# Performance work log

Measured on AMD Instinct MI355X. Metric: run time of the kernel, lower is better.

Reference implementation:

```python
import jax, jax.numpy as jnp
import numpy as np

# Model constants (match init_kwargs)
H = 256          # hidden_dim
NH = 4           # num_heads
L = 4            # gnn_layers
T = 4            # transformer_layers
KMAX = 10        # k_max for overlap embedding
MAXD = 32        # MAX_DIST
INC = 119        # in_channels (atom vocab)
ED = 5           # edge_dim (bond vocab)
B = 64           # graphs per batch
M_SUB = 32       # subgraphs per graph (m)
KNODE = 32       # nodes per subgraph (k)
S = B * M_SUB    # total subgraphs = 2048
N = S * KNODE    # flattened nodes = 65536
E = 131072       # intra-subgraph directed edges


def _ln(x, g, b):
    mu = x.mean(-1, keepdims=True)
    var = ((x - mu) ** 2).mean(-1, keepdims=True)
    return (x - mu) * jax.lax.rsqrt(var + 1e-5) * g + b


def setup_inputs() -> dict:
    key = jax.random.key(0)
    ks = iter(jax.random.split(key, 24))
    nk = lambda: next(ks)
    rn = lambda k_, shp: 0.02 * jax.random.normal(k_, shp, dtype=jnp.float32)

    x_ids = jax.random.randint(nk(), (N,), 0, INC)
    edge_ids = jax.random.randint(nk(), (E,), 0, ED)
    # intra-subgraph edges: endpoints stay within each block of KNODE nodes
    eps_per = E // S
    base = jnp.repeat(jnp.arange(S) * KNODE, eps_per)
    src = base + jax.random.randint(nk(), (E,), 0, KNODE)
    dst = base + jax.random.randint(nk(), (E,), 0, KNODE)
    ns = jax.random.randint(nk(), (S, KNODE), 0, 500)
    padm = jax.random.uniform(nk(), (S, KNODE)) < 0.1
    nodes_sampled = jnp.where(padm, -1, ns)
    dist = jax.random.randint(nk(), (N,), 0, MAXD + 1)
    lp = -5.0 * jax.random.uniform(nk(), (S,))

    return {
        'x_ids': x_ids, 'edge_ids': edge_ids, 'src': src, 'dst': dst,
        'nodes_sampled': nodes_sampled, 'dist': dist, 'lp': lp,
        'atom_emb': rn(nk(), (INC, H)), 'bond_emb': rn(nk(), (ED, H)),
        'dist_emb': rn(nk(), (MAXD + 1, H)),
        'logp_W': rn(nk(), (H,)), 'logp_b': jnp.zeros((H,)),
        'gnn_eps': jnp.zeros((L,)),
        'gnn_W1': rn(nk(), (L, H, H)), 'gnn_b1': jnp.zeros((L, H)),
        'gnn_W2': rn(nk(), (L, H, H)), 'gnn_b2': jnp.zeros((L, H)),
        'ln1_g': jnp.ones((T, H)), 'ln1_b': jnp.zeros((T, H)),
        'qkv_W': rn(nk(), (T, H, 3 * H)),
        'out_W': rn(nk(), (T, H, H)), 'out_b': jnp.zeros((T, H)),
        'ln2_g': jnp.ones((T, H)), 'ln2_b': jnp.zeros((T, H)),
        'f1_W': rn(nk(), (T, H, 4 * H)), 'f1_b': jnp.zeros((T, 4 * H)),
        'f2_W': rn(nk(), (T, 4 * H, H)), 'f2_b': jnp.zeros((T, H)),
        'lnout_g': jnp.ones((H,)), 'lnout_b': jnp.zeros((H,)),
        'overlap_emb': rn(nk(), (KMAX + 1,)),
        'ht_alpha': jnp.ones(()),
    }


def reference(x_ids, edge_ids, src, dst, nodes_sampled, dist, lp,
              atom_emb, bond_emb, dist_emb, logp_W, logp_b,
              gnn_eps, gnn_W1, gnn_b1, gnn_W2, gnn_b2,
              ln1_g, ln1_b, qkv_W, out_W, out_b, ln2_g, ln2_b,
              f1_W, f1_b, f2_W, f2_b, lnout_g, lnout_b,
              overlap_emb, ht_alpha):
    # ---- flatten / embed node features ----
    valid = (nodes_sampled >= 0).reshape(N)
    valid_f = valid.astype(jnp.float32)[:, None]
    lp = jnp.where(jnp.isfinite(lp), lp, 0.0)
    sub_batch = jnp.arange(N) // KNODE
    dist_c = jnp.clip(dist, 0, MAXD)
    logp_pe = jax.nn.relu(lp[sub_batch][:, None] * logp_W + logp_b)
    h = (atom_emb[x_ids] + dist_emb[dist_c] + logp_pe) * valid_f  # [N,H]
    e = bond_emb[edge_ids]                                        # [E,H]

    # ---- GINE message passing ----
    for l in range(L):
        msg = jax.nn.relu(h[src] + e)                       # [E,H] gather
        agg = jax.ops.segment_sum(msg, dst, num_segments=N) # [N,H] scatter-add
        z = (1.0 + gnn_eps[l]) * h + agg
        z = jax.nn.relu(z @ gnn_W1[l] + gnn_b1[l])
        h = (z @ gnn_W2[l] + gnn_b2[l]) * valid_f

    # ---- pool roots into [B, m, H] tokens ----
    root = jnp.arange(S) * KNODE
    x = h[root].reshape(B, M_SUB, H)
    lp2 = lp.reshape(B, M_SUB)

    # ---- pairwise subgraph overlap bias ----
    nodes = nodes_sampled.reshape(B, M_SUB, KNODE)
    vmask = nodes >= 0
    # eq[b,i,j,ki,kj]: node ki of subgraph i equals node kj of subgraph j
    eq = nodes[:, :, None, :, None] == nodes[:, None, :, None, :]
    overlap = (eq.any(-1) & vmask[:, :, None, :]).sum(-1)  # [B,m,m]
    lp_c = jnp.clip(lp2, -30.0, 0.0)
    bias = overlap_emb[jnp.clip(overlap, 0, KMAX)] - ht_alpha * lp_c[:, None, :]
    bias = bias[:, None]  # [B,1,m,m], broadcast over heads

    # ---- relative-bias transformer ----
    hd = H // NH
    scale = 1.0 / np.sqrt(hd).astype(np.float32)
    for t in range(T):
        r = _ln(x, ln1_g[t], ln1_b[t])
        q, k_, v = jnp.split(r @ qkv_W[t], 3, axis=-1)
        q = q.reshape(B, M_SUB, NH, hd)
        k_ = k_.reshape(B, M_SUB, NH, hd)
        v = v.reshape(B, M_SUB, NH, hd)
        scores = jnp.einsum('bihd,bjhd->bhij', q, k_) * scale + bias
        attn = jax.nn.softmax(scores, axis=-1)
        o = jnp.einsum('bhij,bjhd->bihd', attn, v).reshape(B, M_SUB, H)
        x = x + o @ out_W[t] + out_b[t]
        r2 = _ln(x, ln2_g[t], ln2_b[t])
        x = x + jax.nn.gelu(r2 @ f1_W[t] + f1_b[t], approximate=False) @ f2_W[t] + f2_b[t]

    x = _ln(x, lnout_g, lnout_b)
    # HT-weighted mean over subgraph tokens
    w = jax.nn.softmax(-lp_c, axis=1)
    return (w[:, :, None] * x).sum(1)  # [B,H]
```

## Files before the change

### kernel.cpp

```cpp
#include <hip/hip_runtime.h>
#include <hip/hip_bf16.h>
#include <math.h>

#define HDIM   256
#define NHEAD  4
#define LLAY   4
#define TLAY   4
#define KMAXC  10
#define MAXD   32
#define BATCH  64
#define MSUB   32
#define KNODE  32
#define SSUB   2048
#define NNODE  65536
#define NEDGE  131072
#define EPSPER 64
#define EDN    5
#define BSTR   264

typedef unsigned short u16;
typedef __attribute__((ext_vector_type(8))) short bf16x8;
typedef __attribute__((ext_vector_type(4))) float f32x4;

__device__ __forceinline__ float us2f(u16 u) {
    union { unsigned int i; float f; } x; x.i = ((unsigned int)u) << 16; return x.f;
}
__device__ __forceinline__ u16 f2us(float v) {
    union { float f; unsigned int i; } x; x.f = v;
    unsigned int u = x.i;
    u += 0x7fffu + ((u >> 16) & 1u);
    return (u16)(u >> 16);
}
__device__ __forceinline__ float finite_or_zero(float v) {
    return (v == v && fabsf(v) <= 3.0e38f) ? v : 0.0f;
}
__device__ __forceinline__ void gll16(const u16* g, u16* l) {
    __builtin_amdgcn_global_load_lds(
        (const __attribute__((address_space(1))) unsigned int*)g,
        (__attribute__((address_space(3))) unsigned int*)l, 16, 0, 0);
}

__global__ __launch_bounds__(256) void k_csr(
    const int* __restrict__ src, const int* __restrict__ dst,
    const int* __restrict__ eid, u16* __restrict__ perm, u16* __restrict__ off)
{
    __shared__ int sL[4][64], dL[4][64], eL[4][64];
    int wave = threadIdx.x >> 6, lane = threadIdx.x & 63;
    int sgi = blockIdx.x * 4 + wave;
    sL[wave][lane] = src[sgi * 64 + lane] - sgi * KNODE;
    dL[wave][lane] = dst[sgi * 64 + lane] - sgi * KNODE;
    eL[wave][lane] = eid[sgi * 64 + lane];
    __syncthreads();
    if (lane < 32) {
        int cnt = 0;
        for (int e = 0; e < 64; ++e) cnt += (dL[wave][e] == lane) ? 1 : 0;
        int incl = cnt;
        #pragma unroll
        for (int d = 1; d < 32; d <<= 1) {
            int v = __shfl_up(incl, d, 64);
            if (lane >= d) incl += v;
        }
        int start = incl - cnt;
        off[sgi * 32 + lane] = (u16)start;
        int pos = start;
        for (int e = 0; e < 64; ++e) {
            if (dL[wave][e] == lane) {
                perm[sgi * 64 + pos] = (u16)((sL[wave][e] << 3) | eL[wave][e]);
                ++pos;
            }
        }
    }
}

__global__ __launch_bounds__(256) void k_wtrans(
    const float* __restrict__ W, u16* __restrict__ WT, int K, int N)
{
    __shared__ float til[32][33];
    int k0 = blockIdx.x * 32, n0 = blockIdx.y * 32, s = blockIdx.z;
    const float* Wb = W + (size_t)s * K * N;
    u16* Tb = WT + (size_t)s * N * K;
    int j = threadIdx.x & 31, i0 = threadIdx.x >> 5;
    #pragma unroll
    for (int it = 0; it < 4; ++it) {
        int i = i0 + it * 8;
        til[i][j] = Wb[(size_t)(k0 + i) * N + n0 + j];
    }
    __syncthreads();
    #pragma unroll
    for (int it = 0; it < 4; ++it) {
        int i = i0 + it * 8;
        Tb[(size_t)(n0 + i) * K + k0 + j] = f2us(til[j][i]);
    }
}

__global__ __launch_bounds__(256, 2) void k_gnn4(
    const int* __restrict__ x_ids, const int* __restrict__ dist,
    const int* __restrict__ nodes, const float* __restrict__ lp,
    const float* __restrict__ atom_emb, const float* __restrict__ dist_emb,
    const float* __restrict__ logp_W, const float* __restrict__ logp_b,
    const u16* __restrict__ perm, const u16* __restrict__ off,
    const float* __restrict__ bond_emb, const float* __restrict__ eps_arr,
    const float* __restrict__ b1a, const float* __restrict__ b2a,
    const u16* __restrict__ W1T, const u16* __restrict__ W2T,
    float* __restrict__ x)
{
    __shared__ __align__(16) unsigned char smem[38912];
    u16*   hz    = (u16*)smem;
    float* bondL = (float*)(smem + 32768);
    u16*   permL = (u16*)(smem + 38048);
    u16*   offL  = (u16*)(smem + 38304);
    float* validL= (float*)(smem + 38432);
    float* epsL  = (float*)(smem + 38688);

    int tid = threadIdx.x, lane = tid & 63, wave = tid >> 6;
    int row0 = blockIdx.x * 64;
    int fr = lane & 15, quad = lane >> 4;

    for (int i = tid; i < EDN * BSTR; i += 256) {
        int r = i / BSTR, c = i - r * BSTR;
        bondL[i] = (c < 256) ? bond_emb[r * 256 + c] : 0.f;
    }
    if (tid < 128) permL[tid] = perm[blockIdx.x * 128 + tid];
    if (tid < 64) {
        offL[tid] = off[blockIdx.x * 64 + tid];
        validL[tid] = (nodes[row0 + tid] >= 0) ? 1.0f : 0.0f;
    }
    if (tid < 4) epsL[tid] = eps_arr[tid];

    {
        int m = tid & 63, qd = tid >> 6;
        int rg = row0 + m;
        float valid = (nodes[rg] >= 0) ? 1.0f : 0.0f;
        float lpv = finite_or_zero(lp[rg >> 5]);
        int dc = dist[rg]; dc = dc < 0 ? 0 : (dc > MAXD ? MAXD : dc);
        int xid = x_ids[rg];
        #pragma unroll
        for (int k = 0; k < 8; ++k) {
            int cc = qd * 8 + k, c = cc * 8;
            float4 a0 = *reinterpret_cast<const float4*>(atom_emb + xid * 256 + c);
            float4 a1 = *reinterpret_cast<const float4*>(atom_emb + xid * 256 + c + 4);
            float4 d0 = *reinterpret_cast<const float4*>(dist_emb + dc * 256 + c);
            float4 d1 = *reinterpret_cast<const float4*>(dist_emb + dc * 256 + c + 4);
            float4 w0 = *reinterpret_cast<const float4*>(logp_W + c);
            float4 w1 = *reinterpret_cast<const float4*>(logp_W + c + 4);
            float4 p0 = *reinterpret_cast<const float4*>(logp_b + c);
            float4 p1 = *reinterpret_cast<const float4*>(logp_b + c + 4);
            union { bf16x8 v; ushort4 h[2]; } o;
            o.h[0] = (ushort4){
                f2us((a0.x + d0.x + fmaxf(lpv * w0.x + p0.x, 0.f)) * valid),
                f2us((a0.y + d0.y + fmaxf(lpv * w0.y + p0.y, 0.f)) * valid),
                f2us((a0.z + d0.z + fmaxf(lpv * w0.z + p0.z, 0.f)) * valid),
                f2us((a0.w + d0.w + fmaxf(lpv * w0.w + p0.w, 0.f)) * valid) };
            o.h[1] = (ushort4){
                f2us((a1.x + d1.x + fmaxf(lpv * w1.x + p1.x, 0.f)) * valid),
                f2us((a1.y + d1.y + fmaxf(lpv * w1.y + p1.y, 0.f)) * valid),
                f2us((a1.z + d1.z + fmaxf(lpv * w1.z + p1.z, 0.f)) * valid),
                f2us((a1.w + d1.w + fmaxf(lpv * w1.w + p1.w, 0.f)) * valid) };
            *reinterpret_cast<bf16x8*>(hz + m * 256 + ((cc ^ (m & 7)) * 8)) = o.v;
        }
    }
    __syncthreads();

    int rl = tid >> 3, g8 = tid & 7;
    for (int l = 0; l < LLAY; ++l) {
        float ep1 = 1.0f + epsL[l];
        for (int p = 0; p < 2; ++p) {
            int row = p * 32 + rl;
            int e0 = offL[p * 32 + rl];
            int e1 = (rl < 31) ? offL[p * 32 + rl + 1] : 64;
            float a[32];
            #pragma unroll
            for (int q = 0; q < 32; ++q) a[q] = 0.f;
            for (int j = e0; j < e1; ++j) {
                int ent = permL[p * 64 + j];
                int sl = p * 32 + (ent >> 3);
                int be = ent & 7;
                #pragma unroll
                for (int q = 0; q < 4; ++q) {
                    int cc = q * 8 + g8;
                    union { bf16x8 v; u16 s[8]; } hv;
                    hv.v = *reinterpret_cast<const bf16x8*>(
                        hz + sl * 256 + ((cc ^ (sl & 7)) * 8));
                    const float* bp = bondL + be * BSTR + cc * 8;
                    float4 bo0 = *reinterpret_cast<const float4*>(bp);
                    float4 bo1 = *reinterpret_cast<const float4*>(bp + 4);
                    a[q*8+0] += fmaxf(us2f(hv.s[0]) + bo0.x, 0.f);
                    a[q*8+1] += fmaxf(us2f(hv.s[1]) + bo0.y, 0.f);
                    a[q*8+2] += fmaxf(us2f(hv.s[2]) + bo0.z, 0.f);
                    a[q*8+3] += fmaxf(us2f(hv.s[3]) + bo0.w, 0.f);
                    a[q*8+4] += fmaxf(us2f(hv.s[4]) + bo1.x, 0.f);
                    a[q*8+5] += fmaxf(us2f(hv.s[5]) + bo1.y, 0.f);
                    a[q*8+6] += fmaxf(us2f(hv.s[6]) + bo1.z, 0.f);
                    a[q*8+7] += fmaxf(us2f(hv.s[7]) + bo1.w, 0.f);
                }
            }
            __syncthreads();
            #pragma unroll
            for (int q = 0; q < 4; ++q) {
                int cc = q * 8 + g8;
                u16* ptr = hz + row * 256 + ((cc ^ (row & 7)) * 8);
                union { bf16x8 v; u16 s[8]; } hv, ov;
                hv.v = *reinterpret_cast<const bf16x8*>(ptr);
                #pragma unroll
                for (int k = 0; k < 8; ++k)
                    ov.s[k] = f2us(ep1 * us2f(hv.s[k]) + a[q * 8 + k]);
                *reinterpret_cast<bf16x8*>(ptr) = ov.v;
            }
        }
        __syncthreads();

        const u16* W1 = W1T + l * 65536;
        const float* b1 = b1a + l * 256;
        bf16x8 wf[4][8];
        #pragma unroll
        for (int i = 0; i < 4; ++i)
            #pragma unroll
            for (int kc = 0; kc < 8; ++kc)
                wf[i][kc] = *reinterpret_cast<const bf16x8*>(
                    W1 + (size_t)(wave * 64 + i * 16 + fr) * 256 + kc * 32 + quad * 8);
        f32x4 acc[4][4];
        #pragma unroll
        for (int i = 0; i < 4; ++i)
            #pragma unroll
            for (int j = 0; j < 4; ++j) acc[i][j] = (f32x4){0.f, 0.f, 0.f, 0.f};
        #pragma unroll
        for (int kc = 0; kc < 8; ++kc) {
            bf16x8 bfv[4];
            #pragma unroll
            for (int j = 0; j < 4; ++j) {
                int m = j * 16 + fr;
                bfv[j] = *reinterpret_cast<const bf16x8*>(hz + m * 256 + (((kc * 4 + quad) ^ (m & 7)) * 8));
            }
            #pragma unroll
            for (int i = 0; i < 4; ++i)
                #pragma unroll
                for (int j = 0; j < 4; ++j)
                    acc[i][j] = __builtin_amdgcn_mfma_f32_16x16x32_bf16(wf[i][kc], bfv[j], acc[i][j], 0, 0, 0);
        }
        __syncthreads();
        #pragma unroll
        for (int i = 0; i < 4; ++i) {
            int n1b = wave * 64 + i * 16 + quad * 4;
            float4 bb = *reinterpret_cast<const float4*>(b1 + n1b);
            #pragma unroll
            for (int j = 0; j < 4; ++j) {
                int m = j * 16 + fr;
                ushort4 o = { f2us(fmaxf(acc[i][j][0] + bb.x, 0.f)),
                              f2us(fmaxf(acc[i][j][1] + bb.y, 0.f)),
                              f2us(fmaxf(acc[i][j][2] + bb.z, 0.f)),
                              f2us(fmaxf(acc[i][j][3] + bb.w, 0.f)) };
                *reinterpret_cast<ushort4*>(hz + m * 256 + (((n1b >> 3) ^ (m & 7)) * 8) + (n1b & 7)) = o;
            }
        }
        __syncthreads();

        const u16* W2 = W2T + l * 65536;
        const float* b2 = b2a + l * 256;
        #pragma unroll
        for (int i = 0; i < 4; ++i)
            #pragma unroll
            for (int kc = 0; kc < 8; ++kc)
                wf[i][kc] = *reinterpret_cast<const bf16x8*>(
                    W2 + (size_t)(wave * 64 + i * 16 + fr) * 256 + kc * 32 + quad * 8);
        #pragma unroll
        for (int i = 0; i < 4; ++i)
            #pragma unroll
            for (int j = 0; j < 4; ++j) acc[i][j] = (f32x4){0.f, 0.f, 0.f, 0.f};
        #pragma unroll
        for (int kc = 0; kc < 8; ++kc) {
            bf16x8 bfv[4];
            #pragma unroll
            for (int j = 0; j < 4; ++j) {
                int m = j * 16 + fr;
                bfv[j] = *reinterpret_cast<const bf16x8*>(hz + m * 256 + (((kc * 4 + quad) ^ (m & 7)) * 8));
            }
            #pragma unroll
            for (int i = 0; i < 4; ++i)
                #pragma unroll
                for (int j = 0; j < 4; ++j)
                    acc[i][j] = __builtin_amdgcn_mfma_f32_16x16x32_bf16(wf[i][kc], bfv[j], acc[i][j], 0, 0, 0);
        }
        __syncthreads();

        if (l < LLAY - 1) {
            #pragma unroll
            for (int i = 0; i < 4; ++i) {
                int n2b = wave * 64 + i * 16 + quad * 4;
                float4 bb = *reinterpret_cast<const float4*>(b2 + n2b);
                #pragma unroll
                for (int j = 0; j < 4; ++j) {
                    int m = j * 16 + fr;
                    float vm = validL[m];
                    ushort4 o = { f2us((acc[i][j][0] + bb.x) * vm),
                                  f2us((acc[i][j][1] + bb.y) * vm),
                                  f2us((acc[i][j][2] + bb.z) * vm),
                                  f2us((acc[i][j][3] + bb.w) * vm) };
                    *reinterpret_cast<ushort4*>(hz + m * 256 + (((n2b >> 3) ^ (m & 7)) * 8) + (n2b & 7)) = o;
                }
            }
            __syncthreads();
        } else {
            if (fr == 0) {
                #pragma unroll
                for (int i = 0; i < 4; ++i) {
                    int n2b = wave * 64 + i * 16 + quad * 4;
                    float4 bb = *reinterpret_cast<const float4*>(b2 + n2b);
                    #pragma unroll
                    for (int jj = 0; jj < 2; ++jj) {
                        int j = jj * 2, m = j * 16;
                        float vm = validL[m];
                        float4 o = { (acc[i][j][0] + bb.x) * vm,
                                     (acc[i][j][1] + bb.y) * vm,
                                     (acc[i][j][2] + bb.z) * vm,
                                     (acc[i][j][3] + bb.w) * vm };
                        *reinterpret_cast<float4*>(
                            x + (size_t)(blockIdx.x * 2 + (m >> 5)) * 256 + n2b) = o;
                    }
                }
            }
        }
    }
}

__global__ __launch_bounds__(1024) void k_bias(
    const int* __restrict__ nodes, const float* __restrict__ lp,
    const float* __restrict__ ovl_emb, const float* __restrict__ alpha_p,
    float* __restrict__ bias)
{
    int b = blockIdx.x, tid = threadIdx.x;
    __shared__ int nd[32][32];
    __shared__ unsigned int bmv[32][17];
    __shared__ float lpc[32];
    __shared__ float emb[16];
    nd[tid >> 5][tid & 31] = nodes[b * 1024 + tid];
    if (tid < 512) bmv[tid >> 4][tid & 15] = 0u;
    if (tid < 32) {
        float l = finite_or_zero(lp[b * 32 + tid]);
        l = l < -30.f ? -30.f : (l > 0.f ? 0.f : l);
        lpc[tid] = l;
    }
    if (tid >= 64 && tid < 64 + KMAXC + 1) emb[tid - 64] = ovl_emb[tid - 64];
    __syncthreads();
    int own = nd[tid >> 5][tid & 31];
    if (own >= 0) atomicOr(&bmv[tid >> 5][own >> 5], 1u << (own & 31));
    __syncthreads();
    int i = tid >> 5, j = tid & 31;
    float alpha = alpha_p[0];
    int cnt = 0;
    #pragma unroll
    for (int k = 0; k < 32; ++k) {
        int nk = nd[i][k];
        if (nk >= 0) cnt += (int)((bmv[j][nk >> 5] >> (nk & 31)) & 1u);
    }
    bias[b * 1024 + tid] = emb[cnt > KMAXC ? KMAXC : cnt] - alpha * lpc[j];
}

__global__ __launch_bounds__(256) void k_gemmA_ln(
    const float* __restrict__ X, const u16* __restrict__ BT,
    const float* __restrict__ ln_g, const float* __restrict__ ln_b,
    const float* __restrict__ bias, u16* __restrict__ C,
    int N, int act)
{
    __shared__ __align__(16) u16 As[32 * 256];
    __shared__ __align__(16) u16 Bs[64 * 256];
    int tid = threadIdx.x, lane = tid & 63, wave = tid >> 6;
    int wm = wave >> 1, wn = wave & 1;
    int bm = blockIdx.y * 32, bn = blockIdx.x * 64;
    int fr = lane & 15, quad = lane >> 4;

    #pragma unroll
    for (int t = 0; t < 8; ++t) {
        int v = t * 4 + wave;
        int r = v * 2 + (lane >> 5);
        int p = lane & 31;
        int cc = p ^ (r & 7);
        gll16(BT + (size_t)(bn + r) * 256 + cc * 8, Bs + v * 512);
    }
    #pragma unroll
    for (int rr = 0; rr < 8; ++rr) {
        int r = wave * 8 + rr;
        float4 xv = *reinterpret_cast<const float4*>(X + (size_t)(bm + r) * 256 + lane * 4);
        float s = xv.x + xv.y + xv.z + xv.w;
        #pragma unroll
        for (int o2 = 32; o2 > 0; o2 >>= 1) s += __shfl_xor(s, o2);
        float mu = s * (1.0f / 256.0f);
        float d0 = xv.x - mu, d1 = xv.y - mu, d2 = xv.z - mu, d3 = xv.w - mu;
        float sq = d0 * d0 + d1 * d1 + d2 * d2 + d3 * d3;
        #pragma unroll
        for (int o2 = 32; o2 > 0; o2 >>= 1) sq += __shfl_xor(sq, o2);
        float rs = rsqrtf(sq * (1.0f / 256.0f) + 1e-5f);
        int c = lane * 4;
        float4 gv = *reinterpret_cast<const float4*>(ln_g + c);
        float4 bv = *reinterpret_cast<const float4*>(ln_b + c);
        ushort4 o = { f2us(d0 * rs * gv.x + bv.x), f2us(d1 * rs * gv.y + bv.y),
                      f2us(d2 * rs * gv.z + bv.z), f2us(d3 * rs * gv.w + bv.w) };
        *reinterpret_cast<ushort4*>(As + r * 256 + (((lane >> 1) ^ (r & 7)) * 8) + (lane & 1) * 4) = o;
    }
    __syncthreads();

    f32x4 acc[2];
    acc[0] = (f32x4){0,0,0,0}; acc[1] = (f32x4){0,0,0,0};
    #pragma unroll
    for (int kc = 0; kc < 8; ++kc) {
        int am = wm * 16 + fr;
        bf16x8 af = *reinterpret_cast<const bf16x8*>(
            As + am * 256 + (((kc * 4 + quad) ^ (am & 7)) * 8));
        bf16x8 bfr[2];
        #pragma unroll
        for (int j = 0; j < 2; ++j) {
            int br = wn * 32 + j * 16 + fr;
            bfr[j] = *reinterpret_cast<const bf16x8*>(
                Bs + br * 256 + (((kc * 4 + quad) ^ (br & 7)) * 8));
        }
        acc[0] = __builtin_amdgcn_mfma_f32_16x16x32_bf16(af, bfr[0], acc[0], 0, 0, 0);
        acc[1] = __builtin_amdgcn_mfma_f32_16x16x32_bf16(af, bfr[1], acc[1], 0, 0, 0);
    }
    int crow0 = bm + wm * 16 + quad * 4;
    int ccol0 = bn + wn * 32 + fr;
    #pragma unroll
    for (int r = 0; r < 4; ++r) {
        int m = crow0 + r;
        #pragma unroll
        for (int j = 0; j < 2; ++j) {
            int n = ccol0 + j * 16;
            float v = acc[j][r];
            if (bias) v += bias[n];
            if (act == 2) v = 0.5f * v * (1.0f + erff(v * 0.70710678118654752f));
            C[(size_t)m * N + n] = f2us(v);
        }
    }
}

__global__ __launch_bounds__(256) void k_gemmB(
    const u16* __restrict__ A, const u16* __restrict__ BT,
    const float* __restrict__ bias, float* __restrict__ Cout,
    const float* __restrict__ resid, int M, int K, int N)
{
    __shared__ __align__(16) u16 As[32 * 256];
    __shared__ __align__(16) u16 Bs[64 * 256];
    int tid = threadIdx.x, lane = tid & 63, wave = tid >> 6;
    int wm = wave >> 1, wn = wave & 1;
    int bm = blockIdx.y * 32, bn = blockIdx.x * 64;
    int fr = lane & 15, quad = lane >> 4;
    int npan = K >> 8;

    f32x4 acc[2];
    acc[0] = (f32x4){0,0,0,0}; acc[1] = (f32x4){0,0,0,0};
    for (int pan = 0; pan < npan; ++pan) {
        if (pan) __syncthreads();
        int kbase = pan * 256;
        #pragma unroll
        for (int t = 0; t < 4; ++t) {
            int v = t * 4 + wave;
            int r = v * 2 + (lane >> 5);
            int p = lane & 31;
            int cc = p ^ (r & 7);
            gll16(A + (size_t)(bm + r) * K + kbase + cc * 8, As + v * 512);
        }
        #pragma unroll
        for (int t = 0; t < 8; ++t) {
            int v = t * 4 + wave;
            int r = v * 2 + (lane >> 5);
            int p = lane & 31;
            int cc = p ^ (r & 7);
            gll16(BT + (size_t)(bn + r) * K + kbase + cc * 8, Bs + v * 512);
        }
        __syncthreads();
        #pragma unroll
        for (int kc = 0; kc < 8; ++kc) {
            int am = wm * 16 + fr;
            bf16x8 af = *reinterpret_cast<const bf16x8*>(
                As + am * 256 + (((kc * 4 + quad) ^ (am & 7)) * 8));
            bf16x8 bfr[2];
            #pragma unroll
            for (int j = 0; j < 2; ++j) {
                int br = wn * 32 + j * 16 + fr;
                bfr[j] = *reinterpret_cast<const bf16x8*>(
                    Bs + br * 256 + (((kc * 4 + quad) ^ (br & 7)) * 8));
            }
            acc[0] = __builtin_amdgcn_mfma_f32_16x16x32_bf16(af, bfr[0], acc[0], 0, 0, 0);
            acc[1] = __builtin_amdgcn_mfma_f32_16x16x32_bf16(af, bfr[1], acc[1], 0, 0, 0);
        }
    }
    int crow0 = bm + wm * 16 + quad * 4;
    int ccol0 = bn + wn * 32 + fr;
    #pragma unroll
    for (int r = 0; r < 4; ++r) {
        int m = crow0 + r;
        #pragma unroll
        for (int j = 0; j < 2; ++j) {
            int n = ccol0 + j * 16;
            Cout[(size_t)m * N + n] = acc[j][r] + bias[n] + resid[(size_t)m * N + n];
        }
    }
}

__global__ __launch_bounds__(256) void k_attn(
    const u16* __restrict__ qkv, const float* __restrict__ bias, u16* __restrict__ o)
{
    int b = blockIdx.x >> 2, hh = blockIdx.x & 3;
    __shared__ float qs[32][65], ks[32][65], vs[32][65];
    __shared__ float sc[32][33];
    int tid = threadIdx.x;
    #pragma unroll
    for (int u = 0; u < 8; ++u) {
        int idx = tid + u * 256;
        int i = idx >> 6, d = idx & 63;
        size_t base = (size_t)(b * 32 + i) * 768;
        qs[i][d] = us2f(qkv[base + hh * 64 + d]);
        ks[i][d] = us2f(qkv[base + 256 + hh * 64 + d]);
        vs[i][d] = us2f(qkv[base + 512 + hh * 64 + d]);
    }
    __syncthreads();
    #pragma unroll
    for (int u = 0; u < 4; ++u) {
        int p = tid + u * 256;
        int i = p >> 5, j = p & 31;
        float s = 0.f;
        #pragma unroll
        for (int d = 0; d < 64; ++d) s += qs[i][d] * ks[j][d];
        sc[i][j] = s * 0.125f + bias[b * 1024 + i * 32 + j];
    }
    __syncthreads();
    if (tid < 32) {
        int i = tid;
        float m = -1e30f;
        for (int j = 0; j < 32; ++j) m = fmaxf(m, sc[i][j]);
        float sum = 0.f;
        for (int j = 0; j < 32; ++j) { float e = expf(sc[i][j] - m); sc[i][j] = e; sum += e; }
        float inv = 1.0f / sum;
        for (int j = 0; j < 32; ++j) sc[i][j] *= inv;
    }
    __syncthreads();
    #pragma unroll
    for (int u = 0; u < 8; ++u) {
        int idx = tid + u * 256;
        int i = idx >> 6, d = idx & 63;
        float a = 0.f;
        #pragma unroll
        for (int j = 0; j < 32; ++j) a += sc[i][j] * vs[j][d];
        o[(size_t)(b * 32 + i) * 256 + hh * 64 + d] = f2us(a);
    }
}

__global__ __launch_bounds__(256) void k_fin(
    const float* __restrict__ x, const float* __restrict__ lp,
    const float* __restrict__ lnout_g, const float* __restrict__ lnout_b,
    float* __restrict__ out)
{
    __shared__ __align__(16) float xlnf[32 * 260];
    __shared__ float wfin[32];
    int tid = threadIdx.x, lane = tid & 63, wave = tid >> 6;
    int b = blockIdx.x;
    #pragma unroll
    for (int rr = 0; rr < 8; ++rr) {
        int row = wave * 8 + rr;
        float4 xv = *reinterpret_cast<const float4*>(x + (size_t)(b * 32 + row) * 256 + lane * 4);
        float s = xv.x + xv.y + xv.z + xv.w;
        #pragma unroll
        for (int o2 = 32; o2 > 0; o2 >>= 1) s += __shfl_xor(s, o2);
        float mu = s * (1.0f / 256.0f);
        float d0 = xv.x - mu, d1 = xv.y - mu, d2 = xv.z - mu, d3 = xv.w - mu;
        float sq = d0 * d0 + d1 * d1 + d2 * d2 + d3 * d3;
        #pragma unroll
        for (int o2 = 32; o2 > 0; o2 >>= 1) sq += __shfl_xor(sq, o2);
        float rs = rsqrtf(sq * (1.0f / 256.0f) + 1e-5f);
        int c = lane * 4;
        float4 gv = *reinterpret_cast<const float4*>(lnout_g + c);
        float4 bv = *reinterpret_cast<const float4*>(lnout_b + c);
        float4 o = { d0 * rs * gv.x + bv.x, d1 * rs * gv.y + bv.y,
                     d2 * rs * gv.z + bv.z, d3 * rs * gv.w + bv.w };
        *reinterpret_cast<float4*>(xlnf + row * 260 + c) = o;
    }
    __syncthreads();
    if (tid == 0) {
        float l2[32];
        float m = -1e30f;
        for (int i = 0; i < 32; ++i) {
            float l = finite_or_zero(lp[b * 32 + i]);
            l = l < -30.f ? -30.f : (l > 0.f ? 0.f : l);
            l2[i] = -l;
            m = fmaxf(m, -l);
        }
        float s = 0.f;
        for (int i = 0; i < 32; ++i) { float e = expf(l2[i] - m); wfin[i] = e; s += e; }
        float inv = 1.0f / s;
        for (int i = 0; i < 32; ++i) wfin[i] *= inv;
    }
    __syncthreads();
    float a = 0.f;
    for (int i = 0; i < 32; ++i) a += wfin[i] * xlnf[i * 260 + tid];
    out[(size_t)b * 256 + tid] = a;
}

extern "C" void kernel_launch(void* const* d_in, const int* in_sizes, int n_in,
                              void* d_out, int out_size, void* d_ws, size_t ws_size,
                              hipStream_t stream)
{
    const int*   x_ids    = (const int*)d_in[0];
    const int*   edge_ids = (const int*)d_in[1];
    const int*   srcp     = (const int*)d_in[2];
    const int*   dstp     = (const int*)d_in[3];
    const int*   nodes    = (const int*)d_in[4];
    const int*   dist     = (const int*)d_in[5];
    const float* lp       = (const float*)d_in[6];
    const float* atom_emb = (const float*)d_in[7];
    const float* bond_emb = (const float*)d_in[8];
    const float* dist_emb = (const float*)d_in[9];
    const float* logp_W   = (const float*)d_in[10];
    const float* logp_b   = (const float*)d_in[11];
    const float* gnn_eps  = (const float*)d_in[12];
    const float* gnn_W1   = (const float*)d_in[13];
    const float* gnn_b1   = (const float*)d_in[14];
    const float* gnn_W2   = (const float*)d_in[15];
    const float* gnn_b2   = (const float*)d_in[16];
    const float* ln1_g    = (const float*)d_in[17];
    const float* ln1_b    = (const float*)d_in[18];
    const float* qkv_W    = (const float*)d_in[19];
    const float* out_W    = (const float*)d_in[20];
    const float* out_b    = (const float*)d_in[21];
    const float* ln2_g    = (const float*)d_in[22];
    const float* ln2_b    = (const float*)d_in[23];
    const float* f1_W     = (const float*)d_in[24];
    const float* f1_b     = (const float*)d_in[25];
    const float* f2_W     = (const float*)d_in[26];
    const float* f2_b     = (const float*)d_in[27];
    const float* lnout_g  = (const float*)d_in[28];
    const float* lnout_b  = (const float*)d_in[29];
    const float* ovl_emb  = (const float*)d_in[30];
    const float* alpha    = (const float*)d_in[31];

    char* ws = (char*)d_ws;
    u16*   gW1T  = (u16*)(ws + 100663296ull);
    u16*   gW2T  = (u16*)(ws + 100663296ull + 524288ull);
    u16*   permW = (u16*)(ws + 100663296ull + 1048576ull);
    u16*   offW  = (u16*)(ws + 100663296ull + 1310720ull);
    u16*   qkvT  = (u16*)(ws + 33554432ull);
    u16*   outT  = (u16*)(ws + 33554432ull + 1572864ull);
    u16*   f1T   = (u16*)(ws + 33554432ull + 2097152ull);
    u16*   f2T   = (u16*)(ws + 33554432ull + 4194304ull);
    u16*   ob    = (u16*)(ws + 33554432ull + 6291456ull);
    float* biasb = (float*)(ws + 33554432ull + 7340032ull);
    u16*   qkvb  = (u16*)(ws + 33554432ull + 7602176ull);
    u16*   ffh   = (u16*)(ws + 33554432ull + 10747904ull);
    float* x     = (float*)(ws + 67108864ull);

    k_csr<<<SSUB / 4, 256, 0, stream>>>(srcp, dstp, edge_ids, permW, offW);
    k_wtrans<<<dim3(8, 8, 4), 256, 0, stream>>>(gnn_W1, gW1T, 256, 256);
    k_wtrans<<<dim3(8, 8, 4), 256, 0, stream>>>(gnn_W2, gW2T, 256, 256);
    k_gnn4<<<NNODE / 64, 256, 0, stream>>>(
        x_ids, dist, nodes, lp, atom_emb, dist_emb, logp_W, logp_b,
        permW, offW, bond_emb, gnn_eps, gnn_b1, gnn_b2, gW1T, gW2T, x);
    k_wtrans<<<dim3(8, 24, 4), 256, 0, stream>>>(qkv_W, qkvT, 256, 768);
    k_wtrans<<<dim3(8, 8, 4), 256, 0, stream>>>(out_W, outT, 256, 256);
    k_wtrans<<<dim3(8, 32, 4), 256, 0, stream>>>(f1_W, f1T, 256, 1024);
    k_wtrans<<<dim3(32, 8, 4), 256, 0, stream>>>(f2_W, f2T, 1024, 256);
    k_bias<<<BATCH, 1024, 0, stream>>>(nodes, lp, ovl_emb, alpha, biasb);
    for (int t = 0; t < TLAY; ++t) {
        k_gemmA_ln<<<dim3(12, 64), 256, 0, stream>>>(
            x, qkvT + (size_t)t * 768 * 256, ln1_g + t * 256, ln1_b + t * 256,
            nullptr, qkvb, 768, 0);
        k_attn<<<BATCH * NHEAD, 256, 0, stream>>>(qkvb, biasb, ob);
        k_gemmB<<<dim3(4, 64), 256, 0, stream>>>(
            ob, outT + (size_t)t * 65536, out_b + t * 256, x, x, SSUB, 256, 256);
        k_gemmA_ln<<<dim3(16, 64), 256, 0, stream>>>(
            x, f1T + (size_t)t * 1024 * 256, ln2_g + t * 256, ln2_b + t * 256,
            f1_b + t * 1024, ffh, 1024, 2);
        k_gemmB<<<dim3(4, 64), 256, 0, stream>>>(
            ffh, f2T + (size_t)t * 256 * 1024, f2_b + t * 256, x, x, SSUB, 1024, 256);
    }
    k_fin<<<BATCH, 256, 0, stream>>>(x, lp, lnout_g, lnout_b, (float*)d_out);
}
```

Baseline: 525.5 us.

## Fuse LayerNorm, QKV projection and attention into one per-head kernel

Replaces the separate LN+QKV GEMM kernel and the attention kernel with a single kernel per (graph, head). Each block normalizes its 32 token rows, computes that head's Q/K/V slice with MFMA straight from global weights, and runs the softmax attention in shared memory. This removes the bf16 qkv round trip through global memory and one launch per layer. In exchange, LayerNorm is recomputed four times per graph (once per head), only 256 blocks are launched, the weight fragments are read from global memory without shared staging, and Q/K/V are no longer rounded to bf16.

```diff
diff --git a/kernel.cpp b/kernel.cpp
--- a/kernel.cpp
+++ b/kernel.cpp
@@ -355,6 +355,117 @@
     bias[b * 1024 + tid] = emb[cnt > KMAXC ? KMAXC : cnt] - alpha * lpc[j];
 }
 
+__global__ __launch_bounds__(256, 2) void k_attn_ln(
+    const float* __restrict__ x, const float* __restrict__ biasb,
+    const float* __restrict__ ln1_g, const float* __restrict__ ln1_b,
+    const u16* __restrict__ qkvT, u16* __restrict__ ob)
+{
+    __shared__ __align__(16) float xf[32 * 260];
+    __shared__ __align__(16) u16 rb[32 * 256];
+    __shared__ __align__(16) float qs[32 * 68];
+    __shared__ __align__(16) float ks[32 * 68];
+    __shared__ __align__(16) float vs[32 * 68];
+    __shared__ float sc[32 * 33];
+    int tid = threadIdx.x, lane = tid & 63, wave = tid >> 6;
+    int b = blockIdx.x >> 2, h = blockIdx.x & 3;
+    int fr = lane & 15, quad = lane >> 4;
+
+    #pragma unroll
+    for (int u = 0; u < 8; ++u) {
+        int v = u * 256 + tid;
+        int i = v >> 6, c = (v & 63) * 4;
+        *reinterpret_cast<float4*>(xf + i * 260 + c) =
+            *reinterpret_cast<const float4*>(x + (size_t)(b * 32 + i) * 256 + c);
+    }
+    __syncthreads();
+    #pragma unroll
+    for (int rr = 0; rr < 8; ++rr) {
+        int row = wave * 8 + rr;
+        float4 xv = *reinterpret_cast<const float4*>(xf + row * 260 + lane * 4);
+        float s = xv.x + xv.y + xv.z + xv.w;
+        #pragma unroll
+        for (int o2 = 32; o2 > 0; o2 >>= 1) s += __shfl_xor(s, o2);
+        float mu = s * (1.0f / 256.0f);
+        float d0 = xv.x - mu, d1 = xv.y - mu, d2 = xv.z - mu, d3 = xv.w - mu;
+        float sq = d0 * d0 + d1 * d1 + d2 * d2 + d3 * d3;
+        #pragma unroll
+        for (int o2 = 32; o2 > 0; o2 >>= 1) sq += __shfl_xor(sq, o2);
+        float rs = rsqrtf(sq * (1.0f / 256.0f) + 1e-5f);
+        int c = lane * 4;
+        float4 gv = *reinterpret_cast<const float4*>(ln1_g + c);
+        float4 bv = *reinterpret_cast<const float4*>(ln1_b + c);
+        ushort4 o = { f2us(d0 * rs * gv.x + bv.x), f2us(d1 * rs * gv.y + bv.y),
+                      f2us(d2 * rs * gv.z + bv.z), f2us(d3 * rs * gv.w + bv.w) };
+        *reinterpret_cast<ushort4*>(rb + row * 256 + (((c >> 3) ^ (row & 7)) * 8) + (c & 7)) = o;
+    }
+    __syncthreads();
+    f32x4 acc[3][2];
+    #pragma unroll
+    for (int i = 0; i < 3; ++i) { acc[i][0] = (f32x4){0,0,0,0}; acc[i][1] = (f32x4){0,0,0,0}; }
+    for (int kc = 0; kc < 8; ++kc) {
+        bf16x8 wf[3], bfv[2];
+        #pragma unroll
+        for (int i = 0; i < 3; ++i) {
+            int nt = wave * 3 + i;
+            int wrow = (nt >> 2) * 256 + h * 64 + (nt & 3) * 16 + fr;
+            wf[i] = *reinterpret_cast<const bf16x8*>(qkvT + (size_t)wrow * 256 + kc * 32 + quad * 8);
+        }
+        #pragma unroll
+        for (int j = 0; j < 2; ++j) {
+            int m = j * 16 + fr;
+            bfv[j] = *reinterpret_cast<const bf16x8*>(rb + m * 256 + (((kc * 4 + quad) ^ (m & 7)) * 8));
+        }
+        #pragma unroll
+        for (int i = 0; i < 3; ++i)
+            #pragma unroll
+            for (int j = 0; j < 2; ++j)
+                acc[i][j] = __builtin_amdgcn_mfma_f32_16x16x32_bf16(wf[i], bfv[j], acc[i][j], 0, 0, 0);
+    }
+    #pragma unroll
+    for (int i = 0; i < 3; ++i) {
+        int nt = wave * 3 + i;
+        int sec = nt >> 2;
+        int nl = (nt & 3) * 16 + quad * 4;
+        float* dst = (sec == 0) ? qs : ((sec == 1) ? ks : vs);
+        #pragma unroll
+        for (int j = 0; j < 2; ++j) {
+            int m = j * 16 + fr;
+            float4 o = { acc[i][j][0], acc[i][j][1], acc[i][j][2], acc[i][j][3] };
+            *reinterpret_cast<float4*>(dst + m * 68 + nl) = o;
+        }
+    }
+    __syncthreads();
+    #pragma unroll
+    for (int u = 0; u < 4; ++u) {
+        int p = tid + u * 256;
+        int i = p >> 5, j = p & 31;
+        float s = 0.f;
+        #pragma unroll
+        for (int d = 0; d < 64; ++d) s += qs[i * 68 + d] * ks[j * 68 + d];
+        sc[i * 33 + j] = s * 0.125f + biasb[b * 1024 + i * 32 + j];
+    }
+    __syncthreads();
+    if (tid < 32) {
+        int i = tid;
+        float m = -1e30f;
+        for (int j = 0; j < 32; ++j) m = fmaxf(m, sc[i * 33 + j]);
+        float sum = 0.f;
+        for (int j = 0; j < 32; ++j) { float e = expf(sc[i * 33 + j] - m); sc[i * 33 + j] = e; sum += e; }
+        float inv = 1.0f / sum;
+        for (int j = 0; j < 32; ++j) sc[i * 33 + j] *= inv;
+    }
+    __syncthreads();
+    #pragma unroll
+    for (int u = 0; u < 8; ++u) {
+        int idx = tid + u * 256;
+        int i = idx >> 6, d = idx & 63;
+        float a = 0.f;
+        #pragma unroll
+        for (int j = 0; j < 32; ++j) a += sc[i * 33 + j] * vs[j * 68 + d];
+        ob[(size_t)(b * 32 + i) * 256 + h * 64 + d] = f2us(a);
+    }
+}
+
 __global__ __launch_bounds__(256) void k_gemmA_ln(
     const float* __restrict__ X, const u16* __restrict__ BT,
     const float* __restrict__ ln_g, const float* __restrict__ ln_b,
@@ -492,54 +603,6 @@
             int n = ccol0 + j * 16;
             Cout[(size_t)m * N + n] = acc[j][r] + bias[n] + resid[(size_t)m * N + n];
         }
-    }
-}
-
-__global__ __launch_bounds__(256) void k_attn(
-    const u16* __restrict__ qkv, const float* __restrict__ bias, u16* __restrict__ o)
-{
-    int b = blockIdx.x >> 2, hh = blockIdx.x & 3;
-    __shared__ float qs[32][65], ks[32][65], vs[32][65];
-    __shared__ float sc[32][33];
-    int tid = threadIdx.x;
-    #pragma unroll
-    for (int u = 0; u < 8; ++u) {
-        int idx = tid + u * 256;
-        int i = idx >> 6, d = idx & 63;
-        size_t base = (size_t)(b * 32 + i) * 768;
-        qs[i][d] = us2f(qkv[base + hh * 64 + d]);
-        ks[i][d] = us2f(qkv[base + 256 + hh * 64 + d]);
-        vs[i][d] = us2f(qkv[base + 512 + hh * 64 + d]);
-    }
-    __syncthreads();
-    #pragma unroll
-    for (int u = 0; u < 4; ++u) {
-        int p = tid + u * 256;
-        int i = p >> 5, j = p & 31;
-        float s = 0.f;
-        #pragma unroll
-        for (int d = 0; d < 64; ++d) s += qs[i][d] * ks[j][d];
-        sc[i][j] = s * 0.125f + bias[b * 1024 + i * 32 + j];
-    }
-    __syncthreads();
-    if (tid < 32) {
-        int i = tid;
-        float m = -1e30f;
-        for (int j = 0; j < 32; ++j) m = fmaxf(m, sc[i][j]);
-        float sum = 0.f;
-        for (int j = 0; j < 32; ++j) { float e = expf(sc[i][j] - m); sc[i][j] = e; sum += e; }
-        float inv = 1.0f / sum;
-        for (int j = 0; j < 32; ++j) sc[i][j] *= inv;
-    }
-    __syncthreads();
-    #pragma unroll
-    for (int u = 0; u < 8; ++u) {
-        int idx = tid + u * 256;
-        int i = idx >> 6, d = idx & 63;
-        float a = 0.f;
-        #pragma unroll
-        for (int j = 0; j < 32; ++j) a += sc[i][j] * vs[j][d];
-        o[(size_t)(b * 32 + i) * 256 + hh * 64 + d] = f2us(a);
     }
 }
 
@@ -641,7 +704,6 @@
     u16*   f2T   = (u16*)(ws + 33554432ull + 4194304ull);
     u16*   ob    = (u16*)(ws + 33554432ull + 6291456ull);
     float* biasb = (float*)(ws + 33554432ull + 7340032ull);
-    u16*   qkvb  = (u16*)(ws + 33554432ull + 7602176ull);
     u16*   ffh   = (u16*)(ws + 33554432ull + 10747904ull);
     float* x     = (float*)(ws + 67108864ull);
 
@@ -657,10 +719,9 @@
     k_wtrans<<<dim3(32, 8, 4), 256, 0, stream>>>(f2_W, f2T, 1024, 256);
     k_bias<<<BATCH, 1024, 0, stream>>>(nodes, lp, ovl_emb, alpha, biasb);
     for (int t = 0; t < TLAY; ++t) {
-        k_gemmA_ln<<<dim3(12, 64), 256, 0, stream>>>(
-            x, qkvT + (size_t)t * 768 * 256, ln1_g + t * 256, ln1_b + t * 256,
-            nullptr, qkvb, 768, 0);
-        k_attn<<<BATCH * NHEAD, 256, 0, stream>>>(qkvb, biasb, ob);
+        k_attn_ln<<<BATCH * NHEAD, 256, 0, stream>>>(
+            x, biasb, ln1_g + t * 256, ln1_b + t * 256,
+            qkvT + (size_t)t * 768 * 256, ob);
         k_gemmB<<<dim3(4, 64), 256, 0, stream>>>(
             ob, outT + (size_t)t * 65536, out_b + t * 256, x, x, SSUB, 256, 256);
         k_gemmA_ln<<<dim3(16, 64), 256, 0, stream>>>(
```

After: 523.1 us. No clear change (-0.5%).
